# Optimization experiments

Hardware: AMD Instinct MI355X
Metric: run time of the kernel (lower is better)

Reference implementation:

```python
import jax, jax.numpy as jnp
import numpy as np


def setup_inputs() -> dict:
    key = jax.random.key(0)
    k1, k2, k3, k4, k5 = jax.random.split(key, 5)
    B, S, H, NL = 256, 128, 768, 2
    return {
        "t_logits": jax.random.normal(k1, (B, NL), dtype=jnp.float32),
        "s_logits": jax.random.normal(k2, (B, NL), dtype=jnp.float32),
        "t_features": jax.random.normal(k3, (B, S, H), dtype=jnp.float32),
        "s_features": jax.random.normal(k4, (B, S, H), dtype=jnp.float32),
        "labels": jax.random.randint(k5, (B,), 0, NL, dtype=jnp.int64),
        "k": 5,
        "temperature": 4,
    }


def reference(t_logits, s_logits, t_features, s_features, labels, k, temperature):
    B = s_features.shape[0]
    D = s_features.shape[1] * s_features.shape[2]  # flattened feature dim S*H
    T = jnp.asarray(temperature, dtype=s_logits.dtype)

    # train_loss: standard cross-entropy computed inside the student model
    logp = jax.nn.log_softmax(s_logits, axis=-1)
    train_loss = -jnp.mean(jnp.take_along_axis(logp, labels[:, None].astype(jnp.int32), axis=1))

    # soft_loss: KL(batchmean) between temperature-softened teacher/student
    soft_targets = jax.nn.softmax(t_logits / T, axis=-1)
    log_probs = jax.nn.log_softmax(s_logits / T, axis=-1)
    soft_loss = jnp.sum(soft_targets * (jnp.log(soft_targets) - log_probs)) / B * T * T

    # distill_loss: per-sample squared distances to label-matched teacher
    # features, take k nearest (self included, dist 0), sum of per-neighbor
    # MSE = sqdist / D.
    tf = t_features.reshape(B, -1)
    sf = s_features.reshape(B, -1)
    # ||s_i - t_j||^2 via GEMM: [B, B]
    sq = (jnp.sum(sf * sf, axis=1)[:, None]
          + jnp.sum(tf * tf, axis=1)[None, :]
          - 2.0 * sf @ tf.T)
    sq = jnp.maximum(sq, 0.0)
    same = labels[:, None] == labels[None, :]
    masked = jnp.where(same, sq, jnp.inf)
    neg_top, _ = jax.lax.top_k(-masked, k)  # k smallest distances per row
    vals = -neg_top
    valid = jnp.isfinite(vals)  # handles groups smaller than k
    distill_loss = jnp.sum(jnp.where(valid, vals, 0.0)) / D

    return train_loss, soft_loss, distill_loss
```

## Files before the change

kernel.cpp:

```cpp
#include <hip/hip_runtime.h>
#include <math.h>


#define TM 128
#define TN 128
#define BK 32
#define LP 40
#define STH (TM * LP)

typedef __attribute__((ext_vector_type(8))) short short8;
typedef __attribute__((ext_vector_type(4))) float f32x4;

__device__ inline unsigned pack_bf16(float a, float b) {
    unsigned ua = __float_as_uint(a), ub = __float_as_uint(b);
    ua = (ua + 0x7fffu + ((ua >> 16) & 1u)) >> 16;
    ub = (ub + 0x7fffu + ((ub >> 16) & 1u)) >> 16;
    return (ua & 0xffffu) | (ub << 16);
}

__device__ inline void barrier_keep_vmem() {
    asm volatile("s_waitcnt lgkmcnt(0)" ::: "memory");
    __builtin_amdgcn_s_barrier();
    asm volatile("" ::: "memory");
}

__global__ __launch_bounds__(256, 3) void gemm_dot_kernel(const float* __restrict__ S,
                                                          const float* __restrict__ T,
                                                          float* __restrict__ part,
                                                          float* __restrict__ spart,
                                                          float* __restrict__ tpart,
                                                          int* __restrict__ counter,
                                                          int B, int K, int KC,
                                                          int mt, int nt, int gz) {
    extern __shared__ __align__(16) unsigned short smem[];

    const int tid   = threadIdx.x;
    const int blk   = blockIdx.x;
    const int tiles = mt * nt;

    if (blk == 0 && tid == 0) *counter = 0;

    int z, mn;
    if ((gz & 7) == 0) {
        const int xcd  = blk & 7;
        const int slot = blk >> 3;
        const int zpx  = gz >> 3;
        mn = slot % tiles;
        z  = xcd * zpx + slot / tiles;
    } else {
        z  = blk / tiles;
        mn = blk % tiles;
    }
    const int i0 = (mn / nt) * TM;
    const int j0 = (mn % nt) * TN;
    const int kbeg  = z * KC;
    const int iters = KC / BK;

    const int lane = tid & 63;
    const int wid  = tid >> 6;
    const int wm   = wid >> 1;
    const int wn   = wid & 1;
    const int l15  = lane & 15;
    const int quad = lane >> 4;

    const int r = tid >> 1;
    const int h = tid & 1;
    int gi = i0 + r; if (gi >= B) gi = B - 1;
    int gj = j0 + r; if (gj >= B) gj = B - 1;
    const float* srcS = S + (size_t)gi * K + kbeg + h * 16;
    const float* srcT = T + (size_t)gj * K + kbeg + h * 16;
    const int woff = r * LP + h * 16;

    int aoff[4], boff[4];
    #pragma unroll
    for (int t = 0; t < 4; ++t) {
        aoff[t] = (wm * 64 + t * 16 + l15) * LP + quad * 8;
        boff[t] = (wn * 64 + t * 16 + l15) * LP + quad * 8;
    }

    const bool doS = ((mn % nt) == 0);
    const bool doT = ((mn / nt) == 0);

    f32x4 acc[4][4] = {};
    float pns = 0.f, pnt = 0.f;

    f32x4 s0 = *(const f32x4*)(srcS + 0);
    f32x4 s1 = *(const f32x4*)(srcS + 4);
    f32x4 s2 = *(const f32x4*)(srcS + 8);
    f32x4 s3 = *(const f32x4*)(srcS + 12);
    f32x4 t0 = *(const f32x4*)(srcT + 0);
    f32x4 t1 = *(const f32x4*)(srcT + 4);
    f32x4 t2 = *(const f32x4*)(srcT + 8);
    f32x4 t3 = *(const f32x4*)(srcT + 12);

    for (int it = 0; it < iters; ++it) {
        unsigned short* As = smem + (it & 1) * 2 * STH;
        unsigned short* Bs = As + STH;

        if (doS)
            pns += s0.x*s0.x + s0.y*s0.y + s0.z*s0.z + s0.w*s0.w
                 + s1.x*s1.x + s1.y*s1.y + s1.z*s1.z + s1.w*s1.w
                 + s2.x*s2.x + s2.y*s2.y + s2.z*s2.z + s2.w*s2.w
                 + s3.x*s3.x + s3.y*s3.y + s3.z*s3.z + s3.w*s3.w;
        if (doT)
            pnt += t0.x*t0.x + t0.y*t0.y + t0.z*t0.z + t0.w*t0.w
                 + t1.x*t1.x + t1.y*t1.y + t1.z*t1.z + t1.w*t1.w
                 + t2.x*t2.x + t2.y*t2.y + t2.z*t2.z + t2.w*t2.w
                 + t3.x*t3.x + t3.y*t3.y + t3.z*t3.z + t3.w*t3.w;
        uint4 pa0 = make_uint4(pack_bf16(s0.x, s0.y), pack_bf16(s0.z, s0.w),
                               pack_bf16(s1.x, s1.y), pack_bf16(s1.z, s1.w));
        uint4 pa1 = make_uint4(pack_bf16(s2.x, s2.y), pack_bf16(s2.z, s2.w),
                               pack_bf16(s3.x, s3.y), pack_bf16(s3.z, s3.w));
        uint4 pb0 = make_uint4(pack_bf16(t0.x, t0.y), pack_bf16(t0.z, t0.w),
                               pack_bf16(t1.x, t1.y), pack_bf16(t1.z, t1.w));
        uint4 pb1 = make_uint4(pack_bf16(t2.x, t2.y), pack_bf16(t2.z, t2.w),
                               pack_bf16(t3.x, t3.y), pack_bf16(t3.z, t3.w));
        *(uint4*)&As[woff]     = pa0;
        *(uint4*)&As[woff + 8] = pa1;
        *(uint4*)&Bs[woff]     = pb0;
        *(uint4*)&Bs[woff + 8] = pb1;

        if (it + 1 < iters) {
            const float* nS = srcS + (it + 1) * BK;
            const float* nT = srcT + (it + 1) * BK;
            s0 = *(const f32x4*)(nS + 0);
            s1 = *(const f32x4*)(nS + 4);
            s2 = *(const f32x4*)(nS + 8);
            s3 = *(const f32x4*)(nS + 12);
            t0 = *(const f32x4*)(nT + 0);
            t1 = *(const f32x4*)(nT + 4);
            t2 = *(const f32x4*)(nT + 8);
            t3 = *(const f32x4*)(nT + 12);
        }

        barrier_keep_vmem();

        short8 bfr[4];
        #pragma unroll
        for (int ni = 0; ni < 4; ++ni)
            bfr[ni] = *(const short8*)&Bs[boff[ni]];
        #pragma unroll
        for (int mi = 0; mi < 4; ++mi) {
            short8 afr = *(const short8*)&As[aoff[mi]];
            #pragma unroll
            for (int ni = 0; ni < 4; ++ni)
                acc[mi][ni] = __builtin_amdgcn_mfma_f32_16x16x32_bf16(
                    afr, bfr[ni], acc[mi][ni], 0, 0, 0);
        }
    }

    float* outp = part + (size_t)z * B * B;
    #pragma unroll
    for (int mi = 0; mi < 4; ++mi) {
        #pragma unroll
        for (int ni = 0; ni < 4; ++ni) {
            #pragma unroll
            for (int rr = 0; rr < 4; ++rr) {
                const int ig = i0 + wm * 64 + mi * 16 + quad * 4 + rr;
                const int jg = j0 + wn * 64 + ni * 16 + l15;
                if (ig < B && jg < B)
                    outp[(size_t)ig * B + jg] = acc[mi][ni][rr];
            }
        }
    }

    if (doS) {
        float v = pns + __shfl_xor(pns, 1, 64);
        if (h == 0 && i0 + r < B) spart[(size_t)z * B + i0 + r] = v;
    }
    if (doT) {
        float v = pnt + __shfl_xor(pnt, 1, 64);
        if (h == 0 && j0 + r < B) tpart[(size_t)z * B + j0 + r] = v;
    }
}

__global__ __launch_bounds__(256) void tail_kernel(const float* __restrict__ part,
                                                   const float* __restrict__ spart,
                                                   const float* __restrict__ tpart,
                                                   const float* __restrict__ t_logits,
                                                   const float* __restrict__ s_logits,
                                                   const int* __restrict__ labels,
                                                   const int* __restrict__ kp,
                                                   const int* __restrict__ tp,
                                                   float* __restrict__ rowsum,
                                                   int* __restrict__ counter,
                                                   float* __restrict__ out,
                                                   int B, int K, int NL, int gz) {
    const int i   = blockIdx.x;
    const int tid = threadIdx.x;
    const size_t BB = (size_t)B * B;

    __shared__ float svals[256];
    __shared__ float rv[256];
    __shared__ int   ri[256];
    __shared__ float red[4];
    __shared__ float snv;
    __shared__ int   lastf;

    float sp = 0.f;
    for (int z = tid; z < gz; z += 256) sp += spart[(size_t)z * B + i];
    #pragma unroll
    for (int off = 32; off > 0; off >>= 1) sp += __shfl_down(sp, off, 64);
    if ((tid & 63) == 0) red[tid >> 6] = sp;
    __syncthreads();
    if (tid == 0) snv = red[0] + red[1] + red[2] + red[3];
    __syncthreads();
    const float sn = snv;

    float v = INFINITY;
    if (tid < B) {
        const float* pp = part + (size_t)i * B + tid;
        const float* tq = tpart + tid;
        float d0=0.f,d1=0.f,d2=0.f,d3=0.f,d4=0.f,d5=0.f,d6=0.f,d7=0.f;
        float tn = 0.f;
        int z = 0;
        for (; z + 8 <= gz; z += 8) {
            d0 += pp[(size_t)(z+0) * BB];
            d1 += pp[(size_t)(z+1) * BB];
            d2 += pp[(size_t)(z+2) * BB];
            d3 += pp[(size_t)(z+3) * BB];
            d4 += pp[(size_t)(z+4) * BB];
            d5 += pp[(size_t)(z+5) * BB];
            d6 += pp[(size_t)(z+6) * BB];
            d7 += pp[(size_t)(z+7) * BB];
            tn += tq[(size_t)(z+0) * B] + tq[(size_t)(z+1) * B]
                + tq[(size_t)(z+2) * B] + tq[(size_t)(z+3) * B]
                + tq[(size_t)(z+4) * B] + tq[(size_t)(z+5) * B]
                + tq[(size_t)(z+6) * B] + tq[(size_t)(z+7) * B];
        }
        float dt = ((d0+d1)+(d2+d3)) + ((d4+d5)+(d6+d7));
        for (; z < gz; ++z) {
            dt += pp[(size_t)z * BB];
            tn += tq[(size_t)z * B];
        }
        if (labels[i] == labels[tid])
            v = fmaxf(sn + tn - 2.0f * dt, 0.0f);
    }
    svals[tid] = v;
    __syncthreads();

    const int k = kp[0];
    float sum = 0.0f;
    for (int it = 0; it < k; ++it) {
        rv[tid] = svals[tid];
        ri[tid] = tid;
        __syncthreads();
        #pragma unroll
        for (int s = 128; s > 0; s >>= 1) {
            if (tid < s) {
                if (rv[tid + s] < rv[tid]) { rv[tid] = rv[tid + s]; ri[tid] = ri[tid + s]; }
            }
            __syncthreads();
        }
        if (tid == 0) {
            if (rv[0] < 3.0e38f) sum += rv[0];
            svals[ri[0]] = INFINITY;
        }
        __syncthreads();
    }

    if (tid == 0) {
        rowsum[i] = sum;
        __threadfence();
        lastf = (atomicAdd(counter, 1) == B - 1) ? 1 : 0;
    }
    __syncthreads();
    if (!lastf) return;

    __threadfence();
    const float Tv = (float)tp[0];
    float rs = (tid < B) ? rowsum[tid] : 0.f;
    float ce = 0.0f, kl = 0.0f;
    for (int s = tid; s < B; s += 256) {
        const float* sl = s_logits + (size_t)s * NL;
        const float* tl = t_logits + (size_t)s * NL;
        float mx = -INFINITY;
        for (int c = 0; c < NL; ++c) mx = fmaxf(mx, sl[c]);
        float se = 0.0f;
        for (int c = 0; c < NL; ++c) se += expf(sl[c] - mx);
        ce += logf(se) + mx - sl[labels[s]];

        float mxs = -INFINITY, mxt = -INFINITY;
        for (int c = 0; c < NL; ++c) {
            mxs = fmaxf(mxs, sl[c] / Tv);
            mxt = fmaxf(mxt, tl[c] / Tv);
        }
        float ses = 0.0f, set = 0.0f;
        for (int c = 0; c < NL; ++c) {
            ses += expf(sl[c] / Tv - mxs);
            set += expf(tl[c] / Tv - mxt);
        }
        float lses = logf(ses) + mxs;
        float lset = logf(set) + mxt;
        for (int c = 0; c < NL; ++c) {
            float lst = tl[c] / Tv - lset;
            float ls  = sl[c] / Tv - lses;
            kl += expf(lst) * (lst - ls);
        }
    }
    #pragma unroll
    for (int off = 32; off > 0; off >>= 1) {
        ce += __shfl_down(ce, off, 64);
        kl += __shfl_down(kl, off, 64);
        rs += __shfl_down(rs, off, 64);
    }
    __shared__ float wce[4], wkl[4], wrs[4];
    if ((tid & 63) == 0) { wce[tid >> 6] = ce; wkl[tid >> 6] = kl; wrs[tid >> 6] = rs; }
    __syncthreads();
    if (tid == 0) {
        out[0] = (wce[0] + wce[1] + wce[2] + wce[3]) / (float)B;
        out[1] = (wkl[0] + wkl[1] + wkl[2] + wkl[3]) / (float)B * Tv * Tv;
        out[2] = (wrs[0] + wrs[1] + wrs[2] + wrs[3]) / (float)K;
    }
}

extern "C" void kernel_launch(void* const* d_in, const int* in_sizes, int n_in,
                              void* d_out, int out_size, void* d_ws, size_t ws_size,
                              hipStream_t stream) {
    const float* t_logits = (const float*)d_in[0];
    const float* s_logits = (const float*)d_in[1];
    const float* t_feat   = (const float*)d_in[2];
    const float* s_feat   = (const float*)d_in[3];
    const int*   labels   = (const int*)d_in[4];
    const int*   kp       = (const int*)d_in[5];
    const int*   tp       = (const int*)d_in[6];
    float* out = (float*)d_out;

    const int B  = in_sizes[4];
    const int NL = in_sizes[0] / B;
    const int K  = in_sizes[2] / B;
    const size_t BB = (size_t)B * B;

    const int mt = (B + TM - 1) / TM;
    const int nt = (B + TN - 1) / TN;

    const size_t avail = ws_size / 4;
    const int cands[] = {192, 128, 96, 64, 48, 32, 24, 16, 12, 8, 6, 4, 2, 1};
    int gz = 1;
    for (int ci = 0; ci < 14; ++ci) {
        const int g = cands[ci];
        if (K % (g * BK) != 0) continue;
        const size_t need = (size_t)g * BB + 2 * (size_t)g * B + B + 1;
        if (need <= avail) { gz = g; break; }
    }
    const int KC = K / gz;

    float* ws      = (float*)d_ws;
    float* part    = ws;
    float* spart   = part + (size_t)gz * BB;
    float* tpart   = spart + (size_t)gz * B;
    float* rowsum  = tpart + (size_t)gz * B;
    int*   counter = (int*)(rowsum + B);

    const int grid = mt * nt * gz;
    const size_t lds_bytes = 2 * 2 * (size_t)STH * sizeof(unsigned short);
    gemm_dot_kernel<<<grid, 256, lds_bytes, stream>>>(s_feat, t_feat, part,
                                                      spart, tpart, counter,
                                                      B, K, KC, mt, nt, gz);

    tail_kernel<<<B, 256, 0, stream>>>(part, spart, tpart, t_logits, s_logits,
                                       labels, kp, tp, rowsum, counter, out,
                                       B, K, NL, gz);
}
```

Measured before the change: 263.4 us.

## Add parallel split-K reduction kernel and unroll GEMM main loop by two

Adds a zred_kernel that reduces the split-K partial dot products and teacher norms into NZG=8 intermediate slices using many blocks, so the tail kernel only sums 8 slices instead of all gz partials serially per row. The GEMM loop is also unrolled by two with a two-stage register prefetch that fixes the LDS buffer index per step, and split counts are restricted to ones giving an even iteration count. This adds a kernel launch and extra workspace traffic, and the restriction may force a smaller gz.

```diff
diff --git a/kernel.cpp b/kernel.cpp
--- a/kernel.cpp
+++ b/kernel.cpp
@@ -7,6 +7,7 @@
 #define BK 32
 #define LP 40
 #define STH (TM * LP)
+#define NZG 8
 
 typedef __attribute__((ext_vector_type(8))) short short8;
 typedef __attribute__((ext_vector_type(4))) float f32x4;
@@ -84,68 +85,81 @@
     f32x4 acc[4][4] = {};
     float pns = 0.f, pnt = 0.f;
 
-    f32x4 s0 = *(const f32x4*)(srcS + 0);
-    f32x4 s1 = *(const f32x4*)(srcS + 4);
-    f32x4 s2 = *(const f32x4*)(srcS + 8);
-    f32x4 s3 = *(const f32x4*)(srcS + 12);
-    f32x4 t0 = *(const f32x4*)(srcT + 0);
-    f32x4 t1 = *(const f32x4*)(srcT + 4);
-    f32x4 t2 = *(const f32x4*)(srcT + 8);
-    f32x4 t3 = *(const f32x4*)(srcT + 12);
-
-    for (int it = 0; it < iters; ++it) {
-        unsigned short* As = smem + (it & 1) * 2 * STH;
-        unsigned short* Bs = As + STH;
-
-        if (doS)
-            pns += s0.x*s0.x + s0.y*s0.y + s0.z*s0.z + s0.w*s0.w
-                 + s1.x*s1.x + s1.y*s1.y + s1.z*s1.z + s1.w*s1.w
-                 + s2.x*s2.x + s2.y*s2.y + s2.z*s2.z + s2.w*s2.w
-                 + s3.x*s3.x + s3.y*s3.y + s3.z*s3.z + s3.w*s3.w;
-        if (doT)
-            pnt += t0.x*t0.x + t0.y*t0.y + t0.z*t0.z + t0.w*t0.w
-                 + t1.x*t1.x + t1.y*t1.y + t1.z*t1.z + t1.w*t1.w
-                 + t2.x*t2.x + t2.y*t2.y + t2.z*t2.z + t2.w*t2.w
-                 + t3.x*t3.x + t3.y*t3.y + t3.z*t3.z + t3.w*t3.w;
-        uint4 pa0 = make_uint4(pack_bf16(s0.x, s0.y), pack_bf16(s0.z, s0.w),
-                               pack_bf16(s1.x, s1.y), pack_bf16(s1.z, s1.w));
-        uint4 pa1 = make_uint4(pack_bf16(s2.x, s2.y), pack_bf16(s2.z, s2.w),
-                               pack_bf16(s3.x, s3.y), pack_bf16(s3.z, s3.w));
-        uint4 pb0 = make_uint4(pack_bf16(t0.x, t0.y), pack_bf16(t0.z, t0.w),
-                               pack_bf16(t1.x, t1.y), pack_bf16(t1.z, t1.w));
-        uint4 pb1 = make_uint4(pack_bf16(t2.x, t2.y), pack_bf16(t2.z, t2.w),
-                               pack_bf16(t3.x, t3.y), pack_bf16(t3.z, t3.w));
-        *(uint4*)&As[woff]     = pa0;
-        *(uint4*)&As[woff + 8] = pa1;
-        *(uint4*)&Bs[woff]     = pb0;
-        *(uint4*)&Bs[woff + 8] = pb1;
-
-        if (it + 1 < iters) {
-            const float* nS = srcS + (it + 1) * BK;
-            const float* nT = srcT + (it + 1) * BK;
-            s0 = *(const f32x4*)(nS + 0);
-            s1 = *(const f32x4*)(nS + 4);
-            s2 = *(const f32x4*)(nS + 8);
-            s3 = *(const f32x4*)(nS + 12);
-            t0 = *(const f32x4*)(nT + 0);
-            t1 = *(const f32x4*)(nT + 4);
-            t2 = *(const f32x4*)(nT + 8);
-            t3 = *(const f32x4*)(nT + 12);
-        }
-
-        barrier_keep_vmem();
-
-        short8 bfr[4];
+    f32x4 pf[2][8];
+    #pragma unroll
+    for (int u = 0; u < 2; ++u) {
+        const float* pS = srcS + u * BK;
+        const float* pT = srcT + u * BK;
+        pf[u][0] = *(const f32x4*)(pS + 0);
+        pf[u][1] = *(const f32x4*)(pS + 4);
+        pf[u][2] = *(const f32x4*)(pS + 8);
+        pf[u][3] = *(const f32x4*)(pS + 12);
+        pf[u][4] = *(const f32x4*)(pT + 0);
+        pf[u][5] = *(const f32x4*)(pT + 4);
+        pf[u][6] = *(const f32x4*)(pT + 8);
+        pf[u][7] = *(const f32x4*)(pT + 12);
+    }
+
+    for (int it = 0; it < iters; it += 2) {
         #pragma unroll
-        for (int ni = 0; ni < 4; ++ni)
-            bfr[ni] = *(const short8*)&Bs[boff[ni]];
-        #pragma unroll
-        for (int mi = 0; mi < 4; ++mi) {
-            short8 afr = *(const short8*)&As[aoff[mi]];
+        for (int u = 0; u < 2; ++u) {
+            const int i2 = it + u;
+            unsigned short* As = smem + u * 2 * STH;
+            unsigned short* Bs = As + STH;
+
+            f32x4 s0 = pf[u][0], s1 = pf[u][1], s2 = pf[u][2], s3 = pf[u][3];
+            f32x4 t0 = pf[u][4], t1 = pf[u][5], t2 = pf[u][6], t3 = pf[u][7];
+
+            if (doS)
+                pns += s0.x*s0.x + s0.y*s0.y + s0.z*s0.z + s0.w*s0.w
+                     + s1.x*s1.x + s1.y*s1.y + s1.z*s1.z + s1.w*s1.w
+                     + s2.x*s2.x + s2.y*s2.y + s2.z*s2.z + s2.w*s2.w
+                     + s3.x*s3.x + s3.y*s3.y + s3.z*s3.z + s3.w*s3.w;
+            if (doT)
+                pnt += t0.x*t0.x + t0.y*t0.y + t0.z*t0.z + t0.w*t0.w
+                     + t1.x*t1.x + t1.y*t1.y + t1.z*t1.z + t1.w*t1.w
+                     + t2.x*t2.x + t2.y*t2.y + t2.z*t2.z + t2.w*t2.w
+                     + t3.x*t3.x + t3.y*t3.y + t3.z*t3.z + t3.w*t3.w;
+            uint4 pa0 = make_uint4(pack_bf16(s0.x, s0.y), pack_bf16(s0.z, s0.w),
+                                   pack_bf16(s1.x, s1.y), pack_bf16(s1.z, s1.w));
+            uint4 pa1 = make_uint4(pack_bf16(s2.x, s2.y), pack_bf16(s2.z, s2.w),
+                                   pack_bf16(s3.x, s3.y), pack_bf16(s3.z, s3.w));
+            uint4 pb0 = make_uint4(pack_bf16(t0.x, t0.y), pack_bf16(t0.z, t0.w),
+                                   pack_bf16(t1.x, t1.y), pack_bf16(t1.z, t1.w));
+            uint4 pb1 = make_uint4(pack_bf16(t2.x, t2.y), pack_bf16(t2.z, t2.w),
+                                   pack_bf16(t3.x, t3.y), pack_bf16(t3.z, t3.w));
+            *(uint4*)&As[woff]     = pa0;
+            *(uint4*)&As[woff + 8] = pa1;
+            *(uint4*)&Bs[woff]     = pb0;
+            *(uint4*)&Bs[woff + 8] = pb1;
+
+            if (i2 + 2 < iters) {
+                const float* nS = srcS + (i2 + 2) * BK;
+                const float* nT = srcT + (i2 + 2) * BK;
+                pf[u][0] = *(const f32x4*)(nS + 0);
+                pf[u][1] = *(const f32x4*)(nS + 4);
+                pf[u][2] = *(const f32x4*)(nS + 8);
+                pf[u][3] = *(const f32x4*)(nS + 12);
+                pf[u][4] = *(const f32x4*)(nT + 0);
+                pf[u][5] = *(const f32x4*)(nT + 4);
+                pf[u][6] = *(const f32x4*)(nT + 8);
+                pf[u][7] = *(const f32x4*)(nT + 12);
+            }
+
+            barrier_keep_vmem();
+
+            short8 bfr[4];
             #pragma unroll
             for (int ni = 0; ni < 4; ++ni)
-                acc[mi][ni] = __builtin_amdgcn_mfma_f32_16x16x32_bf16(
-                    afr, bfr[ni], acc[mi][ni], 0, 0, 0);
+                bfr[ni] = *(const short8*)&Bs[boff[ni]];
+            #pragma unroll
+            for (int mi = 0; mi < 4; ++mi) {
+                short8 afr = *(const short8*)&As[aoff[mi]];
+                #pragma unroll
+                for (int ni = 0; ni < 4; ++ni)
+                    acc[mi][ni] = __builtin_amdgcn_mfma_f32_16x16x32_bf16(
+                        afr, bfr[ni], acc[mi][ni], 0, 0, 0);
+            }
         }
     }
 
@@ -174,9 +188,48 @@
     }
 }
 
-__global__ __launch_bounds__(256) void tail_kernel(const float* __restrict__ part,
+__global__ __launch_bounds__(256) void zred_kernel(const float* __restrict__ part,
+                                                   const float* __restrict__ tpart,
+                                                   float* __restrict__ dsq2,
+                                                   float* __restrict__ tpart2,
+                                                   int B, int gz) {
+    const int blk = blockIdx.x;
+    const int tid = threadIdx.x;
+    const size_t BB = (size_t)B * B;
+    const int cgrp  = (int)(BB / 256);
+    const int chunk = (gz + NZG - 1) / NZG;
+
+    if (blk < NZG * cgrp) {
+        const int zs = blk / cgrp;
+        const int c  = blk % cgrp;
+        const size_t elem = (size_t)c * 256 + tid;
+        const int z0 = zs * chunk;
+        int z1 = z0 + chunk; if (z1 > gz) z1 = gz;
+        float a0 = 0.f, a1 = 0.f, a2 = 0.f, a3 = 0.f;
+        int z = z0;
+        for (; z + 4 <= z1; z += 4) {
+            a0 += part[(size_t)(z + 0) * BB + elem];
+            a1 += part[(size_t)(z + 1) * BB + elem];
+            a2 += part[(size_t)(z + 2) * BB + elem];
+            a3 += part[(size_t)(z + 3) * BB + elem];
+        }
+        for (; z < z1; ++z) a0 += part[(size_t)z * BB + elem];
+        dsq2[(size_t)zs * BB + elem] = (a0 + a1) + (a2 + a3);
+    } else {
+        const int zs = blk - NZG * cgrp;
+        if (tid < B) {
+            const int z0 = zs * chunk;
+            int z1 = z0 + chunk; if (z1 > gz) z1 = gz;
+            float a = 0.f;
+            for (int z = z0; z < z1; ++z) a += tpart[(size_t)z * B + tid];
+            tpart2[(size_t)zs * B + tid] = a;
+        }
+    }
+}
+
+__global__ __launch_bounds__(256) void tail_kernel(const float* __restrict__ dsq2,
                                                    const float* __restrict__ spart,
-                                                   const float* __restrict__ tpart,
+                                                   const float* __restrict__ tpart2,
                                                    const float* __restrict__ t_logits,
                                                    const float* __restrict__ s_logits,
                                                    const int* __restrict__ labels,
@@ -209,29 +262,11 @@
 
     float v = INFINITY;
     if (tid < B) {
-        const float* pp = part + (size_t)i * B + tid;
-        const float* tq = tpart + tid;
-        float d0=0.f,d1=0.f,d2=0.f,d3=0.f,d4=0.f,d5=0.f,d6=0.f,d7=0.f;
-        float tn = 0.f;
-        int z = 0;
-        for (; z + 8 <= gz; z += 8) {
-            d0 += pp[(size_t)(z+0) * BB];
-            d1 += pp[(size_t)(z+1) * BB];
-            d2 += pp[(size_t)(z+2) * BB];
-            d3 += pp[(size_t)(z+3) * BB];
-            d4 += pp[(size_t)(z+4) * BB];
-            d5 += pp[(size_t)(z+5) * BB];
-            d6 += pp[(size_t)(z+6) * BB];
-            d7 += pp[(size_t)(z+7) * BB];
-            tn += tq[(size_t)(z+0) * B] + tq[(size_t)(z+1) * B]
-                + tq[(size_t)(z+2) * B] + tq[(size_t)(z+3) * B]
-                + tq[(size_t)(z+4) * B] + tq[(size_t)(z+5) * B]
-                + tq[(size_t)(z+6) * B] + tq[(size_t)(z+7) * B];
-        }
-        float dt = ((d0+d1)+(d2+d3)) + ((d4+d5)+(d6+d7));
-        for (; z < gz; ++z) {
-            dt += pp[(size_t)z * BB];
-            tn += tq[(size_t)z * B];
+        float dt = 0.f, tn = 0.f;
+        #pragma unroll
+        for (int zs = 0; zs < NZG; ++zs) {
+            dt += dsq2[(size_t)zs * BB + (size_t)i * B + tid];
+            tn += tpart2[(size_t)zs * B + tid];
         }
         if (labels[i] == labels[tid])
             v = fmaxf(sn + tn - 2.0f * dt, 0.0f);
@@ -340,7 +375,9 @@
     for (int ci = 0; ci < 14; ++ci) {
         const int g = cands[ci];
         if (K % (g * BK) != 0) continue;
-        const size_t need = (size_t)g * BB + 2 * (size_t)g * B + B + 1;
+        if (((K / (g * BK)) & 1) != 0) continue;
+        const size_t need = (size_t)g * BB + 2 * (size_t)g * B + B + 1
+                          + (size_t)NZG * BB + (size_t)NZG * B;
         if (need <= avail) { gz = g; break; }
     }
     const int KC = K / gz;
@@ -351,6 +388,8 @@
     float* tpart   = spart + (size_t)gz * B;
     float* rowsum  = tpart + (size_t)gz * B;
     int*   counter = (int*)(rowsum + B);
+    float* dsq2    = (float*)(counter + 1);
+    float* tpart2  = dsq2 + (size_t)NZG * BB;
 
     const int grid = mt * nt * gz;
     const size_t lds_bytes = 2 * 2 * (size_t)STH * sizeof(unsigned short);
@@ -358,7 +397,11 @@
                                                       spart, tpart, counter,
                                                       B, K, KC, mt, nt, gz);
 
-    tail_kernel<<<B, 256, 0, stream>>>(part, spart, tpart, t_logits, s_logits,
+    const int cgrp  = (int)(BB / 256);
+    const int zgrid = NZG * cgrp + NZG;
+    zred_kernel<<<zgrid, 256, 0, stream>>>(part, tpart, dsq2, tpart2, B, gz);
+
+    tail_kernel<<<B, 256, 0, stream>>>(dsq2, spart, tpart2, t_logits, s_logits,
                                        labels, kp, tp, rowsum, counter, out,
                                        B, K, NL, gz);
 }
```

Result: slower. 274.6 us (+4.2%).

## Widen GEMM tile to 128x256 with 512 threads to reuse student rows

Applied to the files above, without the earlier changes.

The distance GEMM moves from 128x128 tiles with 4 waves to 128x256 tiles with 8 waves in a 2x4 layout. Each student row is now packed once per K-slice and reused across all 256 teacher columns, which cuts redundant global fp32 reads and bf16 packing. The norm reductions and the split-K candidate list are adjusted to match, and shared memory becomes a static array. In exchange each block holds more LDS (about 61 KB), which limits how many blocks fit per CU, and the grid has fewer, larger blocks.

```diff
diff --git a/kernel.cpp b/kernel.cpp
--- a/kernel.cpp
+++ b/kernel.cpp
@@ -2,11 +2,13 @@
 #include <math.h>
 
 
-#define TM 128
-#define TN 128
+#define TMS 128
+#define TNT 256
 #define BK 32
 #define LP 40
-#define STH (TM * LP)
+#define STHS (TMS * LP)
+#define STHT (TNT * LP)
+#define STAGE (STHS + STHT)
 
 typedef __attribute__((ext_vector_type(8))) short short8;
 typedef __attribute__((ext_vector_type(4))) float f32x4;
@@ -24,7 +26,7 @@
     asm volatile("" ::: "memory");
 }
 
-__global__ __launch_bounds__(256, 3) void gemm_dot_kernel(const float* __restrict__ S,
+__global__ __launch_bounds__(512, 4) void gemm_dot_kernel(const float* __restrict__ S,
                                                           const float* __restrict__ T,
                                                           float* __restrict__ part,
                                                           float* __restrict__ spart,
@@ -32,7 +34,7 @@
                                                           int* __restrict__ counter,
                                                           int B, int K, int KC,
                                                           int mt, int nt, int gz) {
-    extern __shared__ __align__(16) unsigned short smem[];
+    __shared__ __align__(16) unsigned short smem[2 * STAGE];
 
     const int tid   = threadIdx.x;
     const int blk   = blockIdx.x;
@@ -51,25 +53,26 @@
         z  = blk / tiles;
         mn = blk % tiles;
     }
-    const int i0 = (mn / nt) * TM;
-    const int j0 = (mn % nt) * TN;
+    const int i0 = (mn / nt) * TMS;
+    const int j0 = (mn % nt) * TNT;
     const int kbeg  = z * KC;
     const int iters = KC / BK;
 
     const int lane = tid & 63;
     const int wid  = tid >> 6;
-    const int wm   = wid >> 1;
-    const int wn   = wid & 1;
+    const int wm   = wid >> 2;
+    const int wn   = wid & 3;
     const int l15  = lane & 15;
     const int quad = lane >> 4;
 
-    const int r = tid >> 1;
-    const int h = tid & 1;
-    int gi = i0 + r; if (gi >= B) gi = B - 1;
-    int gj = j0 + r; if (gj >= B) gj = B - 1;
-    const float* srcS = S + (size_t)gi * K + kbeg + h * 16;
-    const float* srcT = T + (size_t)gj * K + kbeg + h * 16;
-    const int woff = r * LP + h * 16;
+    const int rS = tid >> 2, hS = tid & 3;
+    const int rT = tid >> 1, hT = tid & 1;
+    int gi = i0 + rS; if (gi >= B) gi = B - 1;
+    int gj = j0 + rT; if (gj >= B) gj = B - 1;
+    const float* srcS = S + (size_t)gi * K + kbeg + hS * 8;
+    const float* srcT = T + (size_t)gj * K + kbeg + hT * 16;
+    const int woffS = rS * LP + hS * 8;
+    const int woffT = rT * LP + hT * 16;
 
     int aoff[4], boff[4];
     #pragma unroll
@@ -84,53 +87,44 @@
     f32x4 acc[4][4] = {};
     float pns = 0.f, pnt = 0.f;
 
-    f32x4 s0 = *(const f32x4*)(srcS + 0);
-    f32x4 s1 = *(const f32x4*)(srcS + 4);
-    f32x4 s2 = *(const f32x4*)(srcS + 8);
-    f32x4 s3 = *(const f32x4*)(srcS + 12);
-    f32x4 t0 = *(const f32x4*)(srcT + 0);
-    f32x4 t1 = *(const f32x4*)(srcT + 4);
-    f32x4 t2 = *(const f32x4*)(srcT + 8);
-    f32x4 t3 = *(const f32x4*)(srcT + 12);
+    f32x4 sA0 = *(const f32x4*)(srcS + 0);
+    f32x4 sA1 = *(const f32x4*)(srcS + 4);
+    f32x4 tB0 = *(const f32x4*)(srcT + 0);
+    f32x4 tB1 = *(const f32x4*)(srcT + 4);
+    f32x4 tB2 = *(const f32x4*)(srcT + 8);
+    f32x4 tB3 = *(const f32x4*)(srcT + 12);
 
     for (int it = 0; it < iters; ++it) {
-        unsigned short* As = smem + (it & 1) * 2 * STH;
-        unsigned short* Bs = As + STH;
+        unsigned short* As = smem + (it & 1) * STAGE;
+        unsigned short* Bs = As + STHS;
 
         if (doS)
-            pns += s0.x*s0.x + s0.y*s0.y + s0.z*s0.z + s0.w*s0.w
-                 + s1.x*s1.x + s1.y*s1.y + s1.z*s1.z + s1.w*s1.w
-                 + s2.x*s2.x + s2.y*s2.y + s2.z*s2.z + s2.w*s2.w
-                 + s3.x*s3.x + s3.y*s3.y + s3.z*s3.z + s3.w*s3.w;
+            pns += sA0.x*sA0.x + sA0.y*sA0.y + sA0.z*sA0.z + sA0.w*sA0.w
+                 + sA1.x*sA1.x + sA1.y*sA1.y + sA1.z*sA1.z + sA1.w*sA1.w;
         if (doT)
-            pnt += t0.x*t0.x + t0.y*t0.y + t0.z*t0.z + t0.w*t0.w
-                 + t1.x*t1.x + t1.y*t1.y + t1.z*t1.z + t1.w*t1.w
-                 + t2.x*t2.x + t2.y*t2.y + t2.z*t2.z + t2.w*t2.w
-                 + t3.x*t3.x + t3.y*t3.y + t3.z*t3.z + t3.w*t3.w;
-        uint4 pa0 = make_uint4(pack_bf16(s0.x, s0.y), pack_bf16(s0.z, s0.w),
-                               pack_bf16(s1.x, s1.y), pack_bf16(s1.z, s1.w));
-        uint4 pa1 = make_uint4(pack_bf16(s2.x, s2.y), pack_bf16(s2.z, s2.w),
-                               pack_bf16(s3.x, s3.y), pack_bf16(s3.z, s3.w));
-        uint4 pb0 = make_uint4(pack_bf16(t0.x, t0.y), pack_bf16(t0.z, t0.w),
-                               pack_bf16(t1.x, t1.y), pack_bf16(t1.z, t1.w));
-        uint4 pb1 = make_uint4(pack_bf16(t2.x, t2.y), pack_bf16(t2.z, t2.w),
-                               pack_bf16(t3.x, t3.y), pack_bf16(t3.z, t3.w));
-        *(uint4*)&As[woff]     = pa0;
-        *(uint4*)&As[woff + 8] = pa1;
-        *(uint4*)&Bs[woff]     = pb0;
-        *(uint4*)&Bs[woff + 8] = pb1;
+            pnt += tB0.x*tB0.x + tB0.y*tB0.y + tB0.z*tB0.z + tB0.w*tB0.w
+                 + tB1.x*tB1.x + tB1.y*tB1.y + tB1.z*tB1.z + tB1.w*tB1.w
+                 + tB2.x*tB2.x + tB2.y*tB2.y + tB2.z*tB2.z + tB2.w*tB2.w
+                 + tB3.x*tB3.x + tB3.y*tB3.y + tB3.z*tB3.z + tB3.w*tB3.w;
+        uint4 pa  = make_uint4(pack_bf16(sA0.x, sA0.y), pack_bf16(sA0.z, sA0.w),
+                               pack_bf16(sA1.x, sA1.y), pack_bf16(sA1.z, sA1.w));
+        uint4 pb0 = make_uint4(pack_bf16(tB0.x, tB0.y), pack_bf16(tB0.z, tB0.w),
+                               pack_bf16(tB1.x, tB1.y), pack_bf16(tB1.z, tB1.w));
+        uint4 pb1 = make_uint4(pack_bf16(tB2.x, tB2.y), pack_bf16(tB2.z, tB2.w),
+                               pack_bf16(tB3.x, tB3.y), pack_bf16(tB3.z, tB3.w));
+        *(uint4*)&As[woffS]     = pa;
+        *(uint4*)&Bs[woffT]     = pb0;
+        *(uint4*)&Bs[woffT + 8] = pb1;
 
         if (it + 1 < iters) {
             const float* nS = srcS + (it + 1) * BK;
             const float* nT = srcT + (it + 1) * BK;
-            s0 = *(const f32x4*)(nS + 0);
-            s1 = *(const f32x4*)(nS + 4);
-            s2 = *(const f32x4*)(nS + 8);
-            s3 = *(const f32x4*)(nS + 12);
-            t0 = *(const f32x4*)(nT + 0);
-            t1 = *(const f32x4*)(nT + 4);
-            t2 = *(const f32x4*)(nT + 8);
-            t3 = *(const f32x4*)(nT + 12);
+            sA0 = *(const f32x4*)(nS + 0);
+            sA1 = *(const f32x4*)(nS + 4);
+            tB0 = *(const f32x4*)(nT + 0);
+            tB1 = *(const f32x4*)(nT + 4);
+            tB2 = *(const f32x4*)(nT + 8);
+            tB3 = *(const f32x4*)(nT + 12);
         }
 
         barrier_keep_vmem();
@@ -165,12 +159,14 @@
     }
 
     if (doS) {
-        float v = pns + __shfl_xor(pns, 1, 64);
-        if (h == 0 && i0 + r < B) spart[(size_t)z * B + i0 + r] = v;
+        float v = pns;
+        v += __shfl_xor(v, 1, 64);
+        v += __shfl_xor(v, 2, 64);
+        if ((tid & 3) == 0 && i0 + rS < B) spart[(size_t)z * B + i0 + rS] = v;
     }
     if (doT) {
         float v = pnt + __shfl_xor(pnt, 1, 64);
-        if (h == 0 && j0 + r < B) tpart[(size_t)z * B + j0 + r] = v;
+        if ((tid & 1) == 0 && j0 + rT < B) tpart[(size_t)z * B + j0 + rT] = v;
     }
 }
 
@@ -331,13 +327,13 @@
     const int K  = in_sizes[2] / B;
     const size_t BB = (size_t)B * B;
 
-    const int mt = (B + TM - 1) / TM;
-    const int nt = (B + TN - 1) / TN;
+    const int mt = (B + TMS - 1) / TMS;
+    const int nt = (B + TNT - 1) / TNT;
 
     const size_t avail = ws_size / 4;
-    const int cands[] = {192, 128, 96, 64, 48, 32, 24, 16, 12, 8, 6, 4, 2, 1};
+    const int cands[] = {256, 192, 128, 96, 64, 48, 32, 24, 16, 12, 8, 6, 4, 2, 1};
     int gz = 1;
-    for (int ci = 0; ci < 14; ++ci) {
+    for (int ci = 0; ci < 15; ++ci) {
         const int g = cands[ci];
         if (K % (g * BK) != 0) continue;
         const size_t need = (size_t)g * BB + 2 * (size_t)g * B + B + 1;
@@ -353,10 +349,9 @@
     int*   counter = (int*)(rowsum + B);
 
     const int grid = mt * nt * gz;
-    const size_t lds_bytes = 2 * 2 * (size_t)STH * sizeof(unsigned short);
-    gemm_dot_kernel<<<grid, 256, lds_bytes, stream>>>(s_feat, t_feat, part,
-                                                      spart, tpart, counter,
-                                                      B, K, KC, mt, nt, gz);
+    gemm_dot_kernel<<<grid, 512, 0, stream>>>(s_feat, t_feat, part,
+                                              spart, tpart, counter,
+                                              B, K, KC, mt, nt, gz);
 
     tail_kernel<<<B, 256, 0, stream>>>(part, spart, tpart, t_logits, s_logits,
                                        labels, kp, tp, rowsum, counter, out,
```

After: 280.9 us. 1.07x slower.
